# Kernel tuning notes

Measured on AMD Instinct MI355X. Metric: run time of the kernel, lower is better.

## Reference

```python
import jax, jax.numpy as jnp
import numpy as np
import math

B, S, D, H = 1, 4096, 512, 8


def setup_inputs() -> dict:
    key = jax.random.key(0)
    ks = jax.random.split(key, 7)
    s = 0.02
    return {
        "queries": jax.random.normal(ks[0], (B, S, D), jnp.float32),
        "keys": jax.random.normal(ks[1], (B, S, D), jnp.float32),
        "values": jax.random.normal(ks[2], (B, S, D), jnp.float32),
        "Wq": jax.random.normal(ks[3], (D, D), jnp.float32) * s,
        "Wk": jax.random.normal(ks[4], (D, D), jnp.float32) * s,
        "Wv": jax.random.normal(ks[5], (D, D), jnp.float32) * s,
        "Wo": jax.random.normal(ks[6], (D, D), jnp.float32) * s,
    }


def _split_heads(x, num_heads):
    # (B, S, D) -> (B*H, S, D/H), matching transpose_qkv
    b, s, d = x.shape
    x = x.reshape(b, s, num_heads, d // num_heads).transpose(0, 2, 1, 3)
    return x.reshape(b * num_heads, s, d // num_heads)


def _merge_heads(x, num_heads):
    # (B*H, S, dh) -> (B, S, D), matching transpose_output
    bh, s, dh = x.shape
    x = x.reshape(bh // num_heads, num_heads, s, dh).transpose(0, 2, 1, 3)
    return x.reshape(bh // num_heads, s, num_heads * dh)


def reference(queries, keys, values, Wq, Wk, Wv, Wo):
    q = _split_heads(queries @ Wq.T, H)  # (B*H, S, dh)
    k = _split_heads(keys @ Wk.T, H)
    v = _split_heads(values @ Wv.T, H)
    dh = q.shape[-1]
    scores = jnp.einsum('bqd,bkd->bqk', q, k) / math.sqrt(dh)  # (B*H, Sq, Sk)
    # NOTE: original torch code applies softmax over dim=0 (the batch*heads axis).
    attn = jax.nn.softmax(scores, axis=0)
    out = jnp.einsum('bqk,bkd->bqd', attn, v)  # dropout p=0 -> identity
    out = _merge_heads(out, H)  # (B, S, D)
    return out @ Wo.T
```

## Files before the change

kernel.cpp:

```cpp
#include <hip/hip_runtime.h>
#include <hip/hip_bf16.h>

constexpr int S_ = 4096;
constexpr int D_ = 512;
constexpr int NJC = 4;

using f32x4 = __attribute__((ext_vector_type(4))) float;
using s16x4 = __attribute__((ext_vector_type(4))) short;
using s16x8 = __attribute__((ext_vector_type(8))) short;
using u16x4 = __attribute__((ext_vector_type(4))) unsigned short;
using u16x8 = __attribute__((ext_vector_type(8))) unsigned short;

__device__ __forceinline__ unsigned short f2bf(float f) {
    union { float f; unsigned u; } v; v.f = f;
    unsigned r = v.u + 0x7FFFu + ((v.u >> 16) & 1u);
    return (unsigned short)(r >> 16);
}

__device__ __forceinline__ unsigned pack_bf16(float lo, float hi) {
    float2 t; t.x = lo; t.y = hi;
    __hip_bfloat162 b = __float22bfloat162_rn(t);
    union { __hip_bfloat162 b; unsigned u; } cv; cv.b = b; return cv.u;
}

__device__ __forceinline__ f32x4 mfma16(s16x4 a, s16x4 b, f32x4 c) {
#if __has_builtin(__builtin_amdgcn_mfma_f32_16x16x16bf16_1k)
    return __builtin_amdgcn_mfma_f32_16x16x16bf16_1k(a, b, c, 0, 0, 0);
#elif __has_builtin(__builtin_amdgcn_mfma_f32_16x16x16_bf16)
    return __builtin_amdgcn_mfma_f32_16x16x16_bf16(a, b, c, 0, 0, 0);
#else
    asm volatile("v_mfma_f32_16x16x16_bf16 %0, %1, %2, %0" : "+v"(c) : "v"(a), "v"(b));
    return c;
#endif
}

template<bool IN_BF16, int OUT_MODE>
__global__ __launch_bounds__(256) void proj_kernel(const void* __restrict__ Xv,
                                                   const float* __restrict__ W,
                                                   void* __restrict__ Yv, float scale) {
    constexpr int BM = 128, BN = 64, BK = 64;
    __shared__ unsigned short Xs[BM][BK + 8];
    __shared__ unsigned short Ws_[BN][BK + 8];
    const int m0 = blockIdx.x * BM;
    const int n0 = blockIdx.y * BN;
    const int tid = threadIdx.x;
    const int lane = tid & 63, w = tid >> 6;
    const int wi = w >> 1, wj = w & 1;
    const int lr = lane & 15, lg = lane >> 4;

    f32x4 acc[4][2] = {};

    for (int kt = 0; kt < D_ / BK; ++kt) {
        const int k0 = kt * BK;
        __syncthreads();
        if (IN_BF16) {
            const unsigned short* X = (const unsigned short*)Xv;
#pragma unroll
            for (int r = 0; r < 4; ++r) {
                int idx = tid + r * 256;
                int row = idx >> 3, c8 = idx & 7;
                u16x8 vv = *(const u16x8*)(X + (size_t)(m0 + row) * D_ + k0 + c8 * 8);
                *(u16x8*)&Xs[row][c8 * 8] = vv;
            }
        } else {
            const float* X = (const float*)Xv;
#pragma unroll
            for (int r = 0; r < 8; ++r) {
                int idx = tid + r * 256;
                int row = idx >> 4, c4 = idx & 15;
                f32x4 vv = *(const f32x4*)(X + (size_t)(m0 + row) * D_ + k0 + c4 * 4);
                u16x4 o;
#pragma unroll
                for (int t = 0; t < 4; ++t) o[t] = f2bf(vv[t]);
                *(u16x4*)&Xs[row][c4 * 4] = o;
            }
        }
#pragma unroll
        for (int r = 0; r < 4; ++r) {
            int idx = tid + r * 256;
            int row = idx >> 4, c4 = idx & 15;
            f32x4 vv = *(const f32x4*)(W + (size_t)(n0 + row) * D_ + k0 + c4 * 4);
            u16x4 o;
#pragma unroll
            for (int t = 0; t < 4; ++t) o[t] = f2bf(vv[t]);
            *(u16x4*)&Ws_[row][c4 * 4] = o;
        }
        __syncthreads();
#pragma unroll
        for (int ks = 0; ks < 2; ++ks) {
            s16x8 a[4], b[2];
#pragma unroll
            for (int mf = 0; mf < 4; ++mf)
                a[mf] = *(const s16x8*)&Xs[wi * 64 + mf * 16 + lr][ks * 32 + lg * 8];
#pragma unroll
            for (int nf = 0; nf < 2; ++nf)
                b[nf] = *(const s16x8*)&Ws_[wj * 32 + nf * 16 + lr][ks * 32 + lg * 8];
#pragma unroll
            for (int mf = 0; mf < 4; ++mf)
#pragma unroll
                for (int nf = 0; nf < 2; ++nf)
                    acc[mf][nf] = __builtin_amdgcn_mfma_f32_16x16x32_bf16(a[mf], b[nf], acc[mf][nf], 0, 0, 0);
        }
    }

    if (OUT_MODE == 1) {
        __syncthreads();
        unsigned short* T = &Xs[0][0] + w * 2304;
#pragma unroll
        for (int mf = 0; mf < 4; ++mf)
#pragma unroll
            for (int nf = 0; nf < 2; ++nf)
#pragma unroll
                for (int r = 0; r < 4; ++r) {
                    int n_loc = nf * 16 + lr;
                    int i_loc = mf * 16 + lg * 4 + r;
                    T[n_loc * 72 + i_loc] = f2bf(acc[mf][nf][r] * scale);
                }
        __syncthreads();
        unsigned short* Y = (unsigned short*)Yv;
#pragma unroll
        for (int rr = 0; rr < 4; ++rr) {
            int chunk = lane + rr * 64;
            int n_loc = chunk >> 3, c8 = chunk & 7;
            u16x8 vv = *(const u16x8*)&T[n_loc * 72 + c8 * 8];
            *(u16x8*)(Y + (size_t)(n0 + wj * 32 + n_loc) * S_ + m0 + wi * 64 + c8 * 8) = vv;
        }
    } else {
#pragma unroll
        for (int mf = 0; mf < 4; ++mf)
#pragma unroll
            for (int nf = 0; nf < 2; ++nf)
#pragma unroll
                for (int r = 0; r < 4; ++r) {
                    int i = m0 + wi * 64 + mf * 16 + lg * 4 + r;
                    int n = n0 + wj * 32 + nf * 16 + lr;
                    float val = acc[mf][nf][r] * scale;
                    if (OUT_MODE == 0) ((unsigned short*)Yv)[(size_t)i * D_ + n] = f2bf(val);
                    else                ((float*)Yv)[(size_t)i * D_ + n] = val;
                }
    }
}

__global__ __launch_bounds__(256, 2) void attn_kernel(const unsigned short* __restrict__ Qp,
                                                      const unsigned short* __restrict__ Kp,
                                                      const unsigned short* __restrict__ VpT,
                                                      float* __restrict__ partial) {
    __shared__ float den[2][4][2][64][4];
    const int bid = blockIdx.x;
    const int rank = (bid & 7) * 64 + (bid >> 3);
    const int jc = rank >> 7;
    const int i0 = (rank & 127) * 32;
    const int tid = threadIdx.x;
    const int lane = tid & 63, w = tid >> 6;
    const int lr = lane & 15, lg = lane >> 4;
    const int kb = w * 128;

    s16x8 q[2][4];
#pragma unroll
    for (int f = 0; f < 2; ++f)
#pragma unroll
        for (int kf = 0; kf < 4; ++kf)
            q[f][kf] = *(const s16x8*)(Qp + (size_t)(i0 + f * 16 + lr) * D_ + kb + kf * 32 + lg * 8);

    f32x4 acc[8][2] = {};

    const int t0 = jc * (S_ / NJC / 16);
    const int t1 = t0 + (S_ / NJC / 16);

    for (int t = t0; t < t1; ++t) {
        const int j0 = t * 16;
        const int slot = t & 1;

        s16x4 vA[8];
#pragma unroll
        for (int df = 0; df < 8; ++df)
            vA[df] = *(const s16x4*)(VpT + (size_t)(kb + df * 16 + lr) * S_ + j0 + lg * 4);
        s16x8 kA[4];
#pragma unroll
        for (int kf = 0; kf < 4; ++kf)
            kA[kf] = *(const s16x8*)(Kp + (size_t)(j0 + lr) * D_ + kb + kf * 32 + lg * 8);

        f32x4 sf[2][2] = {};
#pragma unroll
        for (int hh = 0; hh < 2; ++hh)
#pragma unroll
            for (int ks = 0; ks < 2; ++ks)
#pragma unroll
                for (int f = 0; f < 2; ++f)
                    sf[hh][f] = __builtin_amdgcn_mfma_f32_16x16x32_bf16(kA[hh * 2 + ks], q[f][hh * 2 + ks], sf[hh][f], 0, 0, 0);

#pragma unroll
        for (int hh = 0; hh < 2; ++hh)
#pragma unroll
            for (int f = 0; f < 2; ++f)
#pragma unroll
                for (int r = 0; r < 4; ++r)
                    sf[hh][f][r] = exp2f(sf[hh][f][r]);
#pragma unroll
        for (int f = 0; f < 2; ++f)
            *(f32x4*)den[slot][w][f][lane] = sf[0][f] + sf[1][f];

        asm volatile("s_waitcnt lgkmcnt(0)\n\ts_barrier" ::: "memory");

        f32x4 dt[2];
#pragma unroll
        for (int f = 0; f < 2; ++f) {
            dt[f] = *(const f32x4*)den[slot][0][f][lane];
#pragma unroll
            for (int wp = 1; wp < 4; ++wp)
                dt[f] += *(const f32x4*)den[slot][wp][f][lane];
        }

        s16x4 pb[2][2];
#pragma unroll
        for (int f = 0; f < 2; ++f) {
            f32x4 rd;
#pragma unroll
            for (int r = 0; r < 4; ++r) rd[r] = __builtin_amdgcn_rcpf(dt[f][r]);
#pragma unroll
            for (int hh = 0; hh < 2; ++hh) {
                union { s16x4 v; uint2 u; } pc;
                pc.u.x = pack_bf16(sf[hh][f][0] * rd[0], sf[hh][f][1] * rd[1]);
                pc.u.y = pack_bf16(sf[hh][f][2] * rd[2], sf[hh][f][3] * rd[3]);
                pb[hh][f] = pc.v;
            }
        }

#pragma unroll
        for (int df = 0; df < 8; ++df)
#pragma unroll
            for (int f = 0; f < 2; ++f)
                acc[df][f] = mfma16(vA[df], pb[df >> 2][f], acc[df][f]);
    }

    float* P = partial + (size_t)jc * D_ * S_;
#pragma unroll
    for (int df = 0; df < 8; ++df)
#pragma unroll
        for (int f = 0; f < 2; ++f)
#pragma unroll
            for (int r = 0; r < 4; ++r)
                P[(size_t)(kb + df * 16 + lg * 4 + r) * S_ + i0 + f * 16 + lr] = acc[df][f][r];
}

__global__ __launch_bounds__(256) void reduceT_kernel(const float* __restrict__ partial,
                                                      unsigned short* __restrict__ ao) {
    __shared__ float T[64][73];
    const int i0 = blockIdx.x * 64;
    const int d0 = blockIdx.y * 64;
    const int tid = threadIdx.x;
    const int dd = tid >> 2, iq = tid & 3;

    f32x4 sum[4] = {};
#pragma unroll
    for (int jc = 0; jc < NJC; ++jc) {
        const float* src = partial + (size_t)jc * D_ * S_ + (size_t)(d0 + dd) * S_ + i0 + iq * 16;
#pragma unroll
        for (int e = 0; e < 4; ++e)
            sum[e] += *(const f32x4*)(src + e * 4);
    }
#pragma unroll
    for (int e = 0; e < 4; ++e)
#pragma unroll
        for (int s = 0; s < 4; ++s)
            T[dd][iq * 16 + e * 4 + s] = sum[e][s];
    __syncthreads();

    const int ir = tid & 63, dq = tid >> 6;
    unsigned short us[16];
#pragma unroll
    for (int kk = 0; kk < 16; ++kk)
        us[kk] = f2bf(T[dq * 16 + kk][ir]);
    unsigned short* dst = ao + (size_t)(i0 + ir) * D_ + d0 + dq * 16;
    *(u16x8*)dst = *(u16x8*)&us[0];
    *(u16x8*)(dst + 8) = *(u16x8*)&us[8];
}

extern "C" void kernel_launch(void* const* d_in, const int* in_sizes, int n_in,
                              void* d_out, int out_size, void* d_ws, size_t ws_size,
                              hipStream_t stream) {
    const float* q  = (const float*)d_in[0];
    const float* k  = (const float*)d_in[1];
    const float* v  = (const float*)d_in[2];
    const float* Wq = (const float*)d_in[3];
    const float* Wk = (const float*)d_in[4];
    const float* Wv = (const float*)d_in[5];
    const float* Wo = (const float*)d_in[6];

    char* ws = (char*)d_ws;
    unsigned short* Qp  = (unsigned short*)(ws);
    unsigned short* Kp  = (unsigned short*)(ws + (4u  << 20));
    unsigned short* VpT = (unsigned short*)(ws + (8u  << 20));
    float*          part= (float*)        (ws + (12u << 20));
    unsigned short* ao  = (unsigned short*)(ws + (44u << 20));

    const float qscale = 0.125f * 1.44269504088896340736f;

    dim3 pb(256);
    dim3 pg(S_ / 128, D_ / 64);
    proj_kernel<false, 0><<<pg, pb, 0, stream>>>(q, Wq, Qp, qscale);
    proj_kernel<false, 0><<<pg, pb, 0, stream>>>(k, Wk, Kp, 1.0f);
    proj_kernel<false, 1><<<pg, pb, 0, stream>>>(v, Wv, VpT, 1.0f);
    attn_kernel<<<dim3(128 * NJC), pb, 0, stream>>>(Qp, Kp, VpT, part);
    reduceT_kernel<<<dim3(S_ / 64, D_ / 64), pb, 0, stream>>>(part, ao);
    proj_kernel<true, 2><<<pg, pb, 0, stream>>>(ao, Wo, (float*)d_out, 1.0f);
}
```

Measured before the change: 234.5 us.

## Store bf16 row-major attention partials, pick split count from workspace, raise MFMA priority

The attention kernel now writes its per-chunk partial outputs as bf16 in row-major (query, dim) layout instead of fp32 transposed. This lets the reduction become a simple vectorized sum with no transpose through shared memory, and it halves partial-buffer traffic. The number of key chunks (split-K factor) is chosen at runtime from the workspace size (8, 4 or 2), which can give more blocks and more parallelism. It also wraps the MFMA sections in s_setprio and issues the K loads before the V loads. Rounding the partials to bf16 before summing adds some precision error.

```diff
diff --git a/kernel.cpp b/kernel.cpp
--- a/kernel.cpp
+++ b/kernel.cpp
@@ -3,7 +3,6 @@
 
 constexpr int S_ = 4096;
 constexpr int D_ = 512;
-constexpr int NJC = 4;
 
 using f32x4 = __attribute__((ext_vector_type(4))) float;
 using s16x4 = __attribute__((ext_vector_type(4))) short;
@@ -15,6 +14,10 @@
     union { float f; unsigned u; } v; v.f = f;
     unsigned r = v.u + 0x7FFFu + ((v.u >> 16) & 1u);
     return (unsigned short)(r >> 16);
+}
+
+__device__ __forceinline__ float bf2f(unsigned short u) {
+    union { unsigned u; float f; } v; v.u = (unsigned)u << 16; return v.f;
 }
 
 __device__ __forceinline__ unsigned pack_bf16(float lo, float hi) {
@@ -144,10 +147,13 @@
 __global__ __launch_bounds__(256, 2) void attn_kernel(const unsigned short* __restrict__ Qp,
                                                       const unsigned short* __restrict__ Kp,
                                                       const unsigned short* __restrict__ VpT,
-                                                      float* __restrict__ partial) {
+                                                      unsigned short* __restrict__ partial,
+                                                      int tpc) {
     __shared__ float den[2][4][2][64][4];
+    const int nblk = gridDim.x;
+    const int cpx = nblk >> 3;
     const int bid = blockIdx.x;
-    const int rank = (bid & 7) * 64 + (bid >> 3);
+    const int rank = (bid & 7) * cpx + (bid >> 3);
     const int jc = rank >> 7;
     const int i0 = (rank & 127) * 32;
     const int tid = threadIdx.x;
@@ -164,23 +170,24 @@
 
     f32x4 acc[8][2] = {};
 
-    const int t0 = jc * (S_ / NJC / 16);
-    const int t1 = t0 + (S_ / NJC / 16);
+    const int t0 = jc * tpc;
+    const int t1 = t0 + tpc;
 
     for (int t = t0; t < t1; ++t) {
         const int j0 = t * 16;
         const int slot = t & 1;
 
+        s16x8 kA[4];
+#pragma unroll
+        for (int kf = 0; kf < 4; ++kf)
+            kA[kf] = *(const s16x8*)(Kp + (size_t)(j0 + lr) * D_ + kb + kf * 32 + lg * 8);
         s16x4 vA[8];
 #pragma unroll
         for (int df = 0; df < 8; ++df)
             vA[df] = *(const s16x4*)(VpT + (size_t)(kb + df * 16 + lr) * S_ + j0 + lg * 4);
-        s16x8 kA[4];
-#pragma unroll
-        for (int kf = 0; kf < 4; ++kf)
-            kA[kf] = *(const s16x8*)(Kp + (size_t)(j0 + lr) * D_ + kb + kf * 32 + lg * 8);
 
         f32x4 sf[2][2] = {};
+        __builtin_amdgcn_s_setprio(1);
 #pragma unroll
         for (int hh = 0; hh < 2; ++hh)
 #pragma unroll
@@ -188,6 +195,7 @@
 #pragma unroll
                 for (int f = 0; f < 2; ++f)
                     sf[hh][f] = __builtin_amdgcn_mfma_f32_16x16x32_bf16(kA[hh * 2 + ks], q[f][hh * 2 + ks], sf[hh][f], 0, 0, 0);
+        __builtin_amdgcn_s_setprio(0);
 
 #pragma unroll
         for (int hh = 0; hh < 2; ++hh)
@@ -226,54 +234,40 @@
             }
         }
 
+        __builtin_amdgcn_s_setprio(1);
 #pragma unroll
         for (int df = 0; df < 8; ++df)
 #pragma unroll
             for (int f = 0; f < 2; ++f)
                 acc[df][f] = mfma16(vA[df], pb[df >> 2][f], acc[df][f]);
+        __builtin_amdgcn_s_setprio(0);
     }
 
-    float* P = partial + (size_t)jc * D_ * S_;
+    unsigned short* P = partial + (size_t)jc * S_ * D_;
 #pragma unroll
     for (int df = 0; df < 8; ++df)
 #pragma unroll
-        for (int f = 0; f < 2; ++f)
-#pragma unroll
-            for (int r = 0; r < 4; ++r)
-                P[(size_t)(kb + df * 16 + lg * 4 + r) * S_ + i0 + f * 16 + lr] = acc[df][f][r];
-}
-
-__global__ __launch_bounds__(256) void reduceT_kernel(const float* __restrict__ partial,
-                                                      unsigned short* __restrict__ ao) {
-    __shared__ float T[64][73];
-    const int i0 = blockIdx.x * 64;
-    const int d0 = blockIdx.y * 64;
-    const int tid = threadIdx.x;
-    const int dd = tid >> 2, iq = tid & 3;
-
-    f32x4 sum[4] = {};
-#pragma unroll
-    for (int jc = 0; jc < NJC; ++jc) {
-        const float* src = partial + (size_t)jc * D_ * S_ + (size_t)(d0 + dd) * S_ + i0 + iq * 16;
-#pragma unroll
-        for (int e = 0; e < 4; ++e)
-            sum[e] += *(const f32x4*)(src + e * 4);
+        for (int f = 0; f < 2; ++f) {
+            union { u16x4 v; uint2 u; } pc;
+            pc.u.x = pack_bf16(acc[df][f][0], acc[df][f][1]);
+            pc.u.y = pack_bf16(acc[df][f][2], acc[df][f][3]);
+            *(u16x4*)(P + (size_t)(i0 + f * 16 + lr) * D_ + kb + df * 16 + lg * 4) = pc.v;
+        }
+}
+
+__global__ __launch_bounds__(256) void reduceN_kernel(const unsigned short* __restrict__ partial,
+                                                      unsigned short* __restrict__ outp, int njc) {
+    size_t base = ((size_t)blockIdx.x * 256 + threadIdx.x) * 8;
+    float s[8] = {};
+    for (int c = 0; c < njc; ++c) {
+        u16x8 vv = *(const u16x8*)(partial + (size_t)c * S_ * D_ + base);
+#pragma unroll
+        for (int e = 0; e < 8; ++e) s[e] += bf2f(vv[e]);
     }
-#pragma unroll
-    for (int e = 0; e < 4; ++e)
-#pragma unroll
-        for (int s = 0; s < 4; ++s)
-            T[dd][iq * 16 + e * 4 + s] = sum[e][s];
-    __syncthreads();
-
-    const int ir = tid & 63, dq = tid >> 6;
-    unsigned short us[16];
-#pragma unroll
-    for (int kk = 0; kk < 16; ++kk)
-        us[kk] = f2bf(T[dq * 16 + kk][ir]);
-    unsigned short* dst = ao + (size_t)(i0 + ir) * D_ + d0 + dq * 16;
-    *(u16x8*)dst = *(u16x8*)&us[0];
-    *(u16x8*)(dst + 8) = *(u16x8*)&us[8];
+    u16x8 o;
+#pragma unroll
+    for (int e = 0; e < 8; ++e) o[e] = f2bf(s[e]);
+    *(u16x8*)(outp + base) = o;
 }
 
 extern "C" void kernel_launch(void* const* d_in, const int* in_sizes, int n_in,
@@ -287,12 +281,16 @@
     const float* Wv = (const float*)d_in[5];
     const float* Wo = (const float*)d_in[6];
 
+    int njc = 2;
+    if      (ws_size >= ((size_t)(16 + 4 * 8) << 20)) njc = 8;
+    else if (ws_size >= ((size_t)(16 + 4 * 4) << 20)) njc = 4;
+
     char* ws = (char*)d_ws;
     unsigned short* Qp  = (unsigned short*)(ws);
     unsigned short* Kp  = (unsigned short*)(ws + (4u  << 20));
     unsigned short* VpT = (unsigned short*)(ws + (8u  << 20));
-    float*          part= (float*)        (ws + (12u << 20));
-    unsigned short* ao  = (unsigned short*)(ws + (44u << 20));
+    unsigned short* part= (unsigned short*)(ws + (12u << 20));
+    unsigned short* ao  = (unsigned short*)(ws + ((size_t)(12 + 4 * njc) << 20));
 
     const float qscale = 0.125f * 1.44269504088896340736f;
 
@@ -301,7 +299,7 @@
     proj_kernel<false, 0><<<pg, pb, 0, stream>>>(q, Wq, Qp, qscale);
     proj_kernel<false, 0><<<pg, pb, 0, stream>>>(k, Wk, Kp, 1.0f);
     proj_kernel<false, 1><<<pg, pb, 0, stream>>>(v, Wv, VpT, 1.0f);
-    attn_kernel<<<dim3(128 * NJC), pb, 0, stream>>>(Qp, Kp, VpT, part);
-    reduceT_kernel<<<dim3(S_ / 64, D_ / 64), pb, 0, stream>>>(part, ao);
+    attn_kernel<<<dim3(128 * njc), pb, 0, stream>>>(Qp, Kp, VpT, part, S_ / 16 / njc);
+    reduceN_kernel<<<dim3(S_ * D_ / 2048), pb, 0, stream>>>(part, ao, njc);
     proj_kernel<true, 2><<<pg, pb, 0, stream>>>(ao, Wo, (float*)d_out, 1.0f);
 }
```

After: 244.1 us. 4.1% more time.
